# Kernel optimization log

Hardware: AMD Instinct MI355X
Metric: run time of the kernel (lower is better)

## Reference

```python
import jax, jax.numpy as jnp
import numpy as np

SAMPLES = 8    # batch of sets
N = 1024       # set size == rows of the permutation-closed index matrix
K = 16         # number of distinct weight-sharing groups
M = N // K     # columns per group per row (rectangular splits)
CI = 128       # channels_in
CO = 256       # channels_out


def setup_inputs() -> dict:
    key = jax.random.key(0)
    kx, kw = jax.random.split(key)
    x = jax.random.normal(kx, (SAMPLES, N, CI), dtype=jnp.float32)
    # weightParameter: [k, channels_out, channels_in]
    W = jax.random.normal(kw, (K, CO, CI), dtype=jnp.float32)
    # Rebuild the circulant group structure that __init__ derives from
    # running_weight_matrix: row j of `indices` is roll(base, j), so the
    # columns of group g in row j are (pos_g + j) mod N.
    base = np.repeat(np.arange(K), M)                      # indices row 0, [N]
    pos = np.stack([np.where(base == g)[0] for g in range(K)])  # [K, M]
    splits = (pos[:, None, :] + np.arange(N)[None, :, None]) % N  # [K, N, M]
    return {"x": x, "W": W, "splits": jnp.asarray(splits, jnp.int32)}


def reference(x, W, splits):
    # sum-pool branch: result = sum_g ( sum_m x[:, splits[g]] ) @ W[g].T
    def body(acc, group):
        w, sp = group                      # w: [CO, CI], sp: [N, M]
        pooled = x[:, sp].sum(axis=2)      # gather [S, N, M, CI] -> [S, N, CI]
        return acc + jnp.einsum('snc,oc->sno', pooled, w), None

    init = jnp.zeros((x.shape[0], splits.shape[1], W.shape[1]), dtype=x.dtype)
    out, _ = jax.lax.scan(body, init, (W, splits))
    return out                             # [S, N, CO]
```

## Files before the change

kernel.cpp:

```cpp
#include <hip/hip_runtime.h>
#include <hip/hip_bf16.h>

#define S_   8
#define N_   1024
#define KG_  16
#define MW_  64
#define CI_  128
#define CO_  256

typedef __attribute__((ext_vector_type(8))) short bf16x8;
typedef __attribute__((ext_vector_type(4))) float f32x4;

__global__ __launch_bounds__(256) void win_kernel(const float* __restrict__ x,
                                                  const float* __restrict__ W,
                                                  __hip_bfloat16* __restrict__ win,
                                                  __hip_bfloat16* __restrict__ Wb) {
    __shared__ float lds[96][CI_];
    const int b   = blockIdx.x;
    const int tid = threadIdx.x;

    {
        const int wi = (b * 256 + tid) * 8;
        const float4 v0 = *(const float4*)&W[wi];
        const float4 v1 = *(const float4*)&W[wi + 4];
        union { unsigned short u[8]; uint4 v; } o;
        __hip_bfloat16 h;
        h = __float2bfloat16(v0.x); o.u[0] = *(unsigned short*)&h;
        h = __float2bfloat16(v0.y); o.u[1] = *(unsigned short*)&h;
        h = __float2bfloat16(v0.z); o.u[2] = *(unsigned short*)&h;
        h = __float2bfloat16(v0.w); o.u[3] = *(unsigned short*)&h;
        h = __float2bfloat16(v1.x); o.u[4] = *(unsigned short*)&h;
        h = __float2bfloat16(v1.y); o.u[5] = *(unsigned short*)&h;
        h = __float2bfloat16(v1.z); o.u[6] = *(unsigned short*)&h;
        h = __float2bfloat16(v1.w); o.u[7] = *(unsigned short*)&h;
        *(uint4*)&Wb[wi] = o.v;
    }

    const int s   = b >> 5;
    const int t0  = (b & 31) << 5;
    const float* xs = x + (size_t)s * N_ * CI_;

    for (int e = tid * 4; e < 96 * CI_; e += 256 * 4) {
        const int r = e >> 7;
        const int c = e & (CI_ - 1);
        *(float4*)&lds[r][c] = *(const float4*)&xs[((t0 + r) & (N_ - 1)) * CI_ + c];
    }
    __syncthreads();

    const int c  = tid & (CI_ - 1);
    const int tb = (tid >> 7) << 4;
    float s0 = 0.f, s1 = 0.f, s2 = 0.f, s3 = 0.f;
    #pragma unroll
    for (int m = 0; m < MW_; m += 4) {
        s0 += lds[tb + m + 0][c];
        s1 += lds[tb + m + 1][c];
        s2 += lds[tb + m + 2][c];
        s3 += lds[tb + m + 3][c];
    }
    float w = (s0 + s1) + (s2 + s3);
    __hip_bfloat16* wo = win + (size_t)s * N_ * CI_;
    wo[(t0 + tb) * CI_ + c] = __float2bfloat16(w);
    #pragma unroll
    for (int t = 1; t < 16; ++t) {
        w += lds[tb + t - 1 + MW_][c] - lds[tb + t - 1][c];
        wo[(t0 + tb + t) * CI_ + c] = __float2bfloat16(w);
    }
}

#define BKE  64
#define AST  (64 * BKE)
#define BST  (64 * BKE)
#define KSTEPS 32

__global__ __launch_bounds__(256, 2) void gemm_kernel(const __hip_bfloat16* __restrict__ winb,
                                                      const __hip_bfloat16* __restrict__ Wb,
                                                      float* __restrict__ out) {
    __shared__ __align__(16) unsigned short Alds[2 * AST];
    __shared__ __align__(16) unsigned short Blds[2 * BST];

    const int tid = threadIdx.x;
    const int l   = tid & 63;
    const int wv  = tid >> 6;
    const int s   = blockIdx.x >> 4;
    const int n0  = (blockIdx.x & 15) << 6;
    const int o0  = blockIdx.y << 6;

    const int wm = wv >> 1;
    const int wn = wv & 1;
    const int fr = l & 15;
    const int kq = l >> 4;
    const int rl = l >> 3;
    const int ps = l & 7;

    const unsigned short* winp = (const unsigned short*)winb + (size_t)s * N_ * CI_;
    const unsigned short* Wp   = (const unsigned short*)Wb;

    f32x4 acc[2][2];
    #pragma unroll
    for (int i = 0; i < 2; ++i)
        #pragma unroll
        for (int j = 0; j < 2; ++j)
            acc[i][j] = f32x4{0.f, 0.f, 0.f, 0.f};

    auto stage = [&](int t, int buf) {
        const int g  = t >> 1;
        const int ch = (t & 1) << 6;
        unsigned short* Ab = &Alds[buf * AST];
        unsigned short* Bb = &Blds[buf * BST];
        #pragma unroll
        for (int q = 0; q < 2; ++q) {
            const int rb  = (wv * 2 + q) * 8;
            const int row = rb + rl;
            const int ss  = ps ^ (row & 7);
            const unsigned short* src =
                winp + (((n0 + (g << 6) + row) & (N_ - 1)) * CI_) + ch + ss * 8;
            __builtin_amdgcn_global_load_lds((const __attribute__((address_space(1))) void*)src,
                                             (__attribute__((address_space(3))) void*)(Ab + rb * BKE),
                                             16, 0, 0);
        }
        #pragma unroll
        for (int q = 0; q < 2; ++q) {
            const int rb  = (wv * 2 + q) * 8;
            const int row = rb + rl;
            const int ss  = ps ^ (row & 7);
            const unsigned short* src =
                Wp + ((g * CO_ + o0 + row) * CI_) + ch + ss * 8;
            __builtin_amdgcn_global_load_lds((const __attribute__((address_space(1))) void*)src,
                                             (__attribute__((address_space(3))) void*)(Bb + rb * BKE),
                                             16, 0, 0);
        }
    };

    stage(0, 0);

    for (int t = 0; t < KSTEPS; ++t) {
        const int cur = t & 1;
        if (t < KSTEPS - 1) {
            stage(t + 1, cur ^ 1);
            asm volatile("s_waitcnt vmcnt(4)" ::: "memory");
        } else {
            asm volatile("s_waitcnt vmcnt(0)" ::: "memory");
        }
        __builtin_amdgcn_sched_barrier(0);
        __builtin_amdgcn_s_barrier();

        const unsigned short* Ab = &Alds[cur * AST];
        const unsigned short* Bb = &Blds[cur * BST];
        #pragma unroll
        for (int ks = 0; ks < 2; ++ks) {
            const int sl = ks * 4 + kq;
            bf16x8 af[2], bfg[2];
            #pragma unroll
            for (int i = 0; i < 2; ++i) {
                const int row = wm * 32 + i * 16 + fr;
                af[i] = *(const bf16x8*)&Ab[row * BKE + ((sl ^ (row & 7)) * 8)];
            }
            #pragma unroll
            for (int j = 0; j < 2; ++j) {
                const int col = wn * 32 + j * 16 + fr;
                bfg[j] = *(const bf16x8*)&Bb[col * BKE + ((sl ^ (col & 7)) * 8)];
            }
            #pragma unroll
            for (int i = 0; i < 2; ++i)
                #pragma unroll
                for (int j = 0; j < 2; ++j)
                    acc[i][j] = __builtin_amdgcn_mfma_f32_16x16x32_bf16(af[i], bfg[j], acc[i][j], 0, 0, 0);
        }
        __builtin_amdgcn_sched_barrier(0);
        __builtin_amdgcn_s_barrier();
    }

    float* op = out + ((size_t)(s * N_ + n0 + wm * 32) * CO_) + o0 + wn * 32;
    #pragma unroll
    for (int i = 0; i < 2; ++i)
        #pragma unroll
        for (int j = 0; j < 2; ++j)
            #pragma unroll
            for (int r = 0; r < 4; ++r)
                op[(i * 16 + kq * 4 + r) * CO_ + j * 16 + fr] = acc[i][j][r];
}

extern "C" void kernel_launch(void* const* d_in, const int* in_sizes, int n_in,
                              void* d_out, int out_size, void* d_ws, size_t ws_size,
                              hipStream_t stream) {
    const float* x = (const float*)d_in[0];
    const float* W = (const float*)d_in[1];

    __hip_bfloat16* winb = (__hip_bfloat16*)d_ws;
    __hip_bfloat16* Wbb  = (__hip_bfloat16*)((char*)d_ws +
                              (size_t)S_ * N_ * CI_ * sizeof(__hip_bfloat16));
    float* out = (float*)d_out;

    win_kernel<<<256, 256, 0, stream>>>(x, W, winb, Wbb);
    gemm_kernel<<<dim3(128, 4), 256, 0, stream>>>(winb, Wbb, out);
}
```

Baseline: 88.04 us.

## Triple-buffer GEMM LDS staging and remap blocks to interleave samples

Moves the GEMM tile loads from double to triple buffering, prefetching two k-steps ahead, and adjusts the vmcnt waits to match the deeper pipeline. Also flattens the grid to 1D with the sample index in the low bits, so neighbouring blocks share the same W slice and output tile positions across samples, which may improve cache reuse. Triple buffering raises LDS use to 48KB per block, which can still fit two blocks per CU but adds rotation bookkeeping.

```diff
diff --git a/kernel.cpp b/kernel.cpp
--- a/kernel.cpp
+++ b/kernel.cpp
@@ -75,15 +75,16 @@
 __global__ __launch_bounds__(256, 2) void gemm_kernel(const __hip_bfloat16* __restrict__ winb,
                                                       const __hip_bfloat16* __restrict__ Wb,
                                                       float* __restrict__ out) {
-    __shared__ __align__(16) unsigned short Alds[2 * AST];
-    __shared__ __align__(16) unsigned short Blds[2 * BST];
+    __shared__ __align__(16) unsigned short Alds[3 * AST];
+    __shared__ __align__(16) unsigned short Blds[3 * BST];
 
     const int tid = threadIdx.x;
     const int l   = tid & 63;
     const int wv  = tid >> 6;
-    const int s   = blockIdx.x >> 4;
-    const int n0  = (blockIdx.x & 15) << 6;
-    const int o0  = blockIdx.y << 6;
+    const int s   = blockIdx.x & 7;
+    const int rem = blockIdx.x >> 3;
+    const int n0  = (rem & 15) << 6;
+    const int o0  = (rem >> 4) << 6;
 
     const int wm = wv >> 1;
     const int wn = wv & 1;
@@ -102,11 +103,9 @@
         for (int j = 0; j < 2; ++j)
             acc[i][j] = f32x4{0.f, 0.f, 0.f, 0.f};
 
-    auto stage = [&](int t, int buf) {
+    auto stage = [&](int t, unsigned short* Ab, unsigned short* Bb) {
         const int g  = t >> 1;
         const int ch = (t & 1) << 6;
-        unsigned short* Ab = &Alds[buf * AST];
-        unsigned short* Bb = &Blds[buf * BST];
         #pragma unroll
         for (int q = 0; q < 2; ++q) {
             const int rb  = (wv * 2 + q) * 8;
@@ -131,12 +130,17 @@
         }
     };
 
-    stage(0, 0);
+    stage(0, Alds,       Blds);
+    stage(1, Alds + AST, Blds + BST);
+
+    int cb = 0;
+    int sb = 2;
 
     for (int t = 0; t < KSTEPS; ++t) {
-        const int cur = t & 1;
-        if (t < KSTEPS - 1) {
-            stage(t + 1, cur ^ 1);
+        if (t + 2 < KSTEPS) {
+            stage(t + 2, Alds + sb * AST, Blds + sb * BST);
+            asm volatile("s_waitcnt vmcnt(8)" ::: "memory");
+        } else if (t == KSTEPS - 2) {
             asm volatile("s_waitcnt vmcnt(4)" ::: "memory");
         } else {
             asm volatile("s_waitcnt vmcnt(0)" ::: "memory");
@@ -144,8 +148,8 @@
         __builtin_amdgcn_sched_barrier(0);
         __builtin_amdgcn_s_barrier();
 
-        const unsigned short* Ab = &Alds[cur * AST];
-        const unsigned short* Bb = &Blds[cur * BST];
+        const unsigned short* Ab = Alds + cb * AST;
+        const unsigned short* Bb = Blds + cb * BST;
         #pragma unroll
         for (int ks = 0; ks < 2; ++ks) {
             const int sl = ks * 4 + kq;
@@ -168,6 +172,9 @@
         }
         __builtin_amdgcn_sched_barrier(0);
         __builtin_amdgcn_s_barrier();
+
+        cb = (cb == 2) ? 0 : cb + 1;
+        sb = (sb == 2) ? 0 : sb + 1;
     }
 
     float* op = out + ((size_t)(s * N_ + n0 + wm * 32) * CO_) + o0 + wn * 32;
@@ -192,5 +199,5 @@
     float* out = (float*)d_out;
 
     win_kernel<<<256, 256, 0, stream>>>(x, W, winb, Wbb);
-    gemm_kernel<<<dim3(128, 4), 256, 0, stream>>>(winb, Wbb, out);
+    gemm_kernel<<<512, 256, 0, stream>>>(winb, Wbb, out);
 }
```

Result: no change. 87.59 us (-0.5%).
